# Kernel optimization log

Measured on AMD Instinct MI355X. Metric: run time of the kernel, lower is better.

The kernel has to match this reference:

```python
import jax, jax.numpy as jnp
import numpy as np

N_NODES = 50000
N_EDGES = 1200000
NODE_DIM = 64
HIDDEN = 64
OUT_DIM = 1
N_LAYERS = 3


def setup_inputs() -> dict:
    key = jax.random.key(0)
    ks = jax.random.split(key, 16)
    inp = {
        "H": jax.random.normal(ks[0], (N_NODES, NODE_DIM), dtype=jnp.float32),
        "edge_index": jax.random.randint(ks[1], (2, N_EDGES), 0, N_NODES, dtype=jnp.int64),
        "E": jax.random.normal(ks[2], (N_EDGES, 16), dtype=jnp.float32),
    }
    # per-layer params: node_encoder (enc) and update_w (upd); weights stored [in, out]
    for i in range(N_LAYERS):
        in_dim = NODE_DIM if i == 0 else HIDDEN
        s = 1.0 / np.sqrt(in_dim)
        inp[f"enc_w{i}"] = jax.random.uniform(ks[3 + 2 * i], (in_dim, HIDDEN), jnp.float32, -s, s)
        inp[f"enc_b{i}"] = jax.random.uniform(ks[4 + 2 * i], (HIDDEN,), jnp.float32, -s, s)
        sh = 1.0 / np.sqrt(HIDDEN)
        inp[f"upd_w{i}"] = jax.random.uniform(ks[9 + 2 * i], (HIDDEN, HIDDEN), jnp.float32, -sh, sh)
        inp[f"upd_b{i}"] = jax.random.uniform(ks[10 + 2 * i], (HIDDEN,), jnp.float32, -sh, sh)
    so = 1.0 / np.sqrt(HIDDEN)
    inp["out_w"] = jax.random.uniform(ks[15], (HIDDEN, OUT_DIM), jnp.float32, -so, so)
    inp["out_b"] = jnp.zeros((OUT_DIM,), jnp.float32)
    return inp


def _gcn_forward(H, edge_index, params):
    u, v = edge_index[0], edge_index[1]
    # symmetric normalization with implicit self-loop degree bump (calc_norm_factor)
    deg = jax.ops.segment_sum(jnp.ones(u.shape[0], H.dtype), u, num_segments=N_NODES) + 1.0
    dis = deg ** -0.5  # deg >= 1, never inf
    norm = dis[u] * dis[v]  # [n_edges]
    for i in range(N_LAYERS):
        enc_w, enc_b, upd_w, upd_b = params[i]
        H = H @ enc_w + enc_b                      # node_encoder
        msgs = norm[:, None] * H[u]                # gather + scale
        agg = jax.ops.segment_sum(msgs, v, num_segments=N_NODES)  # scatter-add
        H = jax.nn.relu((agg + H) @ upd_w + upd_b)  # update + ReLU (dropout = identity in eval)
    return H


def reference(H, edge_index, E, enc_w0, enc_b0, upd_w0, upd_b0, enc_w1, enc_b1,
              upd_w1, upd_b1, enc_w2, enc_b2, upd_w2, upd_b2, out_w, out_b):
    params = [(enc_w0, enc_b0, upd_w0, upd_b0),
              (enc_w1, enc_b1, upd_w1, upd_b1),
              (enc_w2, enc_b2, upd_w2, upd_b2)]
    Hf = _gcn_forward(H, edge_index, params)
    graph_emb = jnp.mean(Hf, axis=0, keepdims=True)  # [1, HIDDEN] readout (batch=None)
    return graph_emb @ out_w + out_b                 # [1, OUT_DIM]
```

## Files before the change

kernel.cpp:

```cpp
#include <hip/hip_runtime.h>
#include <hip/hip_fp16.h>

#define NN 50000
#define NE 1200000
#define DIM 64
#define NB 782
#define SLICES 512
#define ES 2344
#define VCAP 2048
#define GB 782
#define FRONT_LDS 33792


__device__ __forceinline__ void lsort_body(char* smem, const int* __restrict__ ei,
                                           ushort* __restrict__ usort,
                                           int* __restrict__ ebuf,
                                           int* __restrict__ lpart_u,
                                           int* __restrict__ lpart_v,
                                           int s) {
    int* hist = (int*)smem;
    int* wsum = (int*)(smem + 3136);
    ushort* sbu = (ushort*)(smem + 4160);
    int* sbv = (int*)(smem + 8848);
    int t = threadIdx.x;
    int w = t >> 6, l = t & 63;
    int e0 = s * ES, e1 = min(e0 + ES, NE), len = e1 - e0;
    int i0 = t * 4;

    int uv[10], vv[10];
#pragma unroll
    for (int j = 0; j < 10; ++j) {
        int e = e0 + t + j * 256;
        uv[j] = (e < e1) ? ei[e] : -1;
        vv[j] = (e < e1) ? ei[NE + e] : -1;
    }

    for (int i = t; i < NB; i += 256) hist[i] = 0;
    __syncthreads();
#pragma unroll
    for (int j = 0; j < 10; ++j)
        if (uv[j] >= 0) atomicAdd(&hist[uv[j] >> 6], 1);
    __syncthreads();
    {
        int h0 = (i0 + 0 < NB) ? hist[i0 + 0] : 0;
        int h1 = (i0 + 1 < NB) ? hist[i0 + 1] : 0;
        int h2 = (i0 + 2 < NB) ? hist[i0 + 2] : 0;
        int h3 = (i0 + 3 < NB) ? hist[i0 + 3] : 0;
        int p1 = h0, p2 = h0 + h1, p3 = p2 + h2, p4 = p3 + h3;
        int inc = p4;
        for (int o = 1; o < 64; o <<= 1) {
            int x = __shfl_up(inc, o, 64);
            if (l >= o) inc += x;
        }
        if (l == 63) wsum[w] = inc;
        __syncthreads();
        int base = 0;
#pragma unroll
        for (int j = 0; j < 4; ++j) if (j < w) base += wsum[j];
        int total = wsum[0] + wsum[1] + wsum[2] + wsum[3];
        int excl = base + inc - p4;
        int* lpu = lpart_u + s * (NB + 1);
        if (i0 + 0 < NB) { lpu[i0 + 0] = excl;      hist[i0 + 0] = excl; }
        if (i0 + 1 < NB) { lpu[i0 + 1] = excl + p1; hist[i0 + 1] = excl + p1; }
        if (i0 + 2 < NB) { lpu[i0 + 2] = excl + p2; hist[i0 + 2] = excl + p2; }
        if (i0 + 3 < NB) { lpu[i0 + 3] = excl + p3; hist[i0 + 3] = excl + p3; }
        if (t == 255) lpu[NB] = total;
    }
    __syncthreads();
#pragma unroll
    for (int j = 0; j < 10; ++j)
        if (uv[j] >= 0) {
            int pos = atomicAdd(&hist[uv[j] >> 6], 1);
            sbu[pos] = (ushort)uv[j];
        }
    __syncthreads();
    for (int i = t; i < len; i += 256) usort[e0 + i] = sbu[i];
    for (int i = t; i < NB; i += 256) hist[i] = 0;
    __syncthreads();

#pragma unroll
    for (int j = 0; j < 10; ++j)
        if (vv[j] >= 0) atomicAdd(&hist[vv[j] >> 6], 1);
    __syncthreads();
    {
        int h0 = (i0 + 0 < NB) ? hist[i0 + 0] : 0;
        int h1 = (i0 + 1 < NB) ? hist[i0 + 1] : 0;
        int h2 = (i0 + 2 < NB) ? hist[i0 + 2] : 0;
        int h3 = (i0 + 3 < NB) ? hist[i0 + 3] : 0;
        int p1 = h0, p2 = h0 + h1, p3 = p2 + h2, p4 = p3 + h3;
        int inc = p4;
        for (int o = 1; o < 64; o <<= 1) {
            int x = __shfl_up(inc, o, 64);
            if (l >= o) inc += x;
        }
        if (l == 63) wsum[w] = inc;
        __syncthreads();
        int base = 0;
#pragma unroll
        for (int j = 0; j < 4; ++j) if (j < w) base += wsum[j];
        int total = wsum[0] + wsum[1] + wsum[2] + wsum[3];
        int excl = base + inc - p4;
        int* lpv = lpart_v + s * (NB + 1);
        if (i0 + 0 < NB) { lpv[i0 + 0] = excl;      hist[i0 + 0] = excl; }
        if (i0 + 1 < NB) { lpv[i0 + 1] = excl + p1; hist[i0 + 1] = excl + p1; }
        if (i0 + 2 < NB) { lpv[i0 + 2] = excl + p2; hist[i0 + 2] = excl + p2; }
        if (i0 + 3 < NB) { lpv[i0 + 3] = excl + p3; hist[i0 + 3] = excl + p3; }
        if (t == 255) lpv[NB] = total;
    }
    __syncthreads();
#pragma unroll
    for (int j = 0; j < 10; ++j)
        if (vv[j] >= 0) {
            int pos = atomicAdd(&hist[vv[j] >> 6], 1);
            sbv[pos] = uv[j] | ((vv[j] & 63) << 16);
        }
    __syncthreads();
    for (int i = t; i < len; i += 256) ebuf[e0 + i] = sbv[i];
}

__device__ __forceinline__ void gemm_h_body(char* smem, int blk,
                                            const float* __restrict__ A,
                                            const float* __restrict__ W,
                                            const float* __restrict__ bias,
                                            __half* __restrict__ Ch, int M) {
    float (*As)[68] = (float(*)[68])smem;
    float (*Bs)[64] = (float(*)[64])(smem + 17408);
    int t = threadIdx.x;
    int row0 = blk * 64;
#pragma unroll
    for (int i = 0; i < 4; ++i) {
        int idx = t + i * 256;
        int r = idx >> 4, c = (idx & 15) << 2;
        float4 val = make_float4(0.f, 0.f, 0.f, 0.f);
        if (row0 + r < M) val = *(const float4*)&A[(size_t)(row0 + r) * DIM + c];
        *(float4*)&As[r][c] = val;
        *(float4*)&Bs[r][c] = *(const float4*)&W[r * DIM + c];
    }
    __syncthreads();
    int r0 = (t >> 4) * 4;
    int c0 = (t & 15) * 4;
    float acc[4][4] = {};
#pragma unroll
    for (int k = 0; k < 64; k += 4) {
        float4 b0 = *(float4*)&Bs[k + 0][c0];
        float4 b1 = *(float4*)&Bs[k + 1][c0];
        float4 b2 = *(float4*)&Bs[k + 2][c0];
        float4 b3 = *(float4*)&Bs[k + 3][c0];
#pragma unroll
        for (int i = 0; i < 4; ++i) {
            float4 av = *(float4*)&As[r0 + i][k];
            acc[i][0] = fmaf(av.x, b0.x, fmaf(av.y, b1.x, fmaf(av.z, b2.x, fmaf(av.w, b3.x, acc[i][0]))));
            acc[i][1] = fmaf(av.x, b0.y, fmaf(av.y, b1.y, fmaf(av.z, b2.y, fmaf(av.w, b3.y, acc[i][1]))));
            acc[i][2] = fmaf(av.x, b0.z, fmaf(av.y, b1.z, fmaf(av.z, b2.z, fmaf(av.w, b3.z, acc[i][2]))));
            acc[i][3] = fmaf(av.x, b0.w, fmaf(av.y, b1.w, fmaf(av.z, b2.w, fmaf(av.w, b3.w, acc[i][3]))));
        }
    }
    float4 bv = *(const float4*)&bias[c0];
#pragma unroll
    for (int i = 0; i < 4; ++i) {
        int r = row0 + r0 + i;
        if (r < M) {
            __half2 p0 = __floats2half2_rn(acc[i][0] + bv.x, acc[i][1] + bv.y);
            __half2 p1 = __floats2half2_rn(acc[i][2] + bv.z, acc[i][3] + bv.w);
            uint2 pk;
            pk.x = *(unsigned int*)&p0;
            pk.y = *(unsigned int*)&p1;
            *(uint2*)&Ch[(size_t)r * DIM + c0] = pk;
        }
    }
}

__global__ __launch_bounds__(256, 2) void k_front(const int* __restrict__ ei,
                                                  ushort* __restrict__ usort,
                                                  int* __restrict__ ebuf,
                                                  int* __restrict__ lpart_u,
                                                  int* __restrict__ lpart_v,
                                                  const float* __restrict__ A,
                                                  const float* __restrict__ W,
                                                  const float* __restrict__ bias,
                                                  __half* __restrict__ Ch) {
    extern __shared__ char smem[];
    int b = blockIdx.x;
    if (b < 256)
        lsort_body(smem, ei, usort, ebuf, lpart_u, lpart_v, b);
    else if (b < 512)
        gemm_h_body(smem, b - 256, A, W, bias, Ch, NN);
    else if (b < 768)
        lsort_body(smem, ei, usort, ebuf, lpart_u, lpart_v, b - 256);
    else
        gemm_h_body(smem, b - 512, A, W, bias, Ch, NN);
}

__global__ __launch_bounds__(256) void k_prep(const ushort* __restrict__ usort,
                                              const int* __restrict__ lpart_u,
                                              const int* __restrict__ ebuf,
                                              const int* __restrict__ lpart_v,
                                              float* __restrict__ dis,
                                              ushort* __restrict__ edges,
                                              int* __restrict__ row_ptr,
                                              float* __restrict__ colsum) {
    __shared__ int cache[VCAP];
    __shared__ int cnt[64];
    __shared__ int cur[64];
    __shared__ int wsum4[4];
    __shared__ int rsum4[4];
    __shared__ int sh[64];
    int bid = blockIdx.x;
    int t = threadIdx.x, w = t >> 6, l = t & 63;
    if (bid < NB) {
        int b = bid;
        if (b == 0 && t < 64) colsum[t] = 0.f;
        if (t < 64) sh[t] = 0;
        __syncthreads();
        for (int s = t; s < SLICES; s += 256) {
            const int* row = lpart_u + s * (NB + 1);
            int st = row[b], en = row[b + 1];
            for (int i = st; i < en; ++i)
                atomicAdd(&sh[usort[s * ES + i] & 63], 1);
        }
        __syncthreads();
        int n = (b << 6) + t;
        if (t < 64 && n < NN) dis[n] = rsqrtf((float)sh[t] + 1.0f);
        return;
    }
    int b = bid - NB;
    int s0 = t * 2, s1 = t * 2 + 1;
    const int* r0p = lpart_v + s0 * (NB + 1);
    const int* r1p = lpart_v + s1 * (NB + 1);
    int a0 = r0p[b], a1 = r0p[b + 1];
    int c0 = r1p[b], c1 = r1p[b + 1];
    int len0 = a1 - a0, len1 = c1 - c0;
    int tl = len0 + len1;
    int ts = a0 + c0;
    int inc = tl;
    for (int o = 1; o < 64; o <<= 1) {
        int x = __shfl_up(inc, o, 64);
        if (l >= o) inc += x;
    }
    int tss = ts;
    for (int off = 32; off; off >>= 1) tss += __shfl_down(tss, off, 64);
    if (l == 63) wsum4[w] = inc;
    if (l == 0) rsum4[w] = tss;
    if (t < 64) cnt[t] = 0;
    __syncthreads();
    int base = 0;
#pragma unroll
    for (int j = 0; j < 4; ++j) if (j < w) base += wsum4[j];
    int n = wsum4[0] + wsum4[1] + wsum4[2] + wsum4[3];
    int rbase = rsum4[0] + rsum4[1] + rsum4[2] + rsum4[3];
    int pos = base + inc - tl;
    if (n <= VCAP) {
        for (int i = 0; i < len0; ++i) cache[pos + i] = ebuf[s0 * ES + a0 + i];
        int pos1 = pos + len0;
        for (int i = 0; i < len1; ++i) cache[pos1 + i] = ebuf[s1 * ES + c0 + i];
        __syncthreads();
        for (int i = t; i < n; i += 256)
            atomicAdd(&cnt[(cache[i] >> 16) & 63], 1);
        __syncthreads();
        if (w == 0) {
            int c = cnt[l];
            int inc2 = c;
            for (int o = 1; o < 64; o <<= 1) {
                int x = __shfl_up(inc2, o, 64);
                if (l >= o) inc2 += x;
            }
            int excl = inc2 - c;
            cur[l] = rbase + excl;
            row_ptr[(b << 6) + l] = rbase + excl;
        }
        __syncthreads();
        for (int i = t; i < n; i += 256) {
            int rec = cache[i];
            int p2 = atomicAdd(&cur[(rec >> 16) & 63], 1);
            edges[p2] = (ushort)(rec & 0xFFFF);
        }
    } else {
        for (int s = t; s < SLICES; s += 256) {
            const int* row = lpart_v + s * (NB + 1);
            int st = row[b], en = row[b + 1];
            for (int i = st; i < en; ++i)
                atomicAdd(&cnt[(ebuf[s * ES + i] >> 16) & 63], 1);
        }
        __syncthreads();
        if (w == 0) {
            int c = cnt[l];
            int inc2 = c;
            for (int o = 1; o < 64; o <<= 1) {
                int x = __shfl_up(inc2, o, 64);
                if (l >= o) inc2 += x;
            }
            int excl = inc2 - c;
            cur[l] = rbase + excl;
            row_ptr[(b << 6) + l] = rbase + excl;
        }
        __syncthreads();
        for (int s = t; s < SLICES; s += 256) {
            const int* row = lpart_v + s * (NB + 1);
            int st = row[b], en = row[b + 1];
            for (int i = st; i < en; ++i) {
                int rec = ebuf[s * ES + i];
                int p2 = atomicAdd(&cur[(rec >> 16) & 63], 1);
                edges[p2] = (ushort)(rec & 0xFFFF);
            }
        }
    }
}

__global__ __launch_bounds__(256) void k_gemm2(const __half* __restrict__ Xh,
                                               const float* __restrict__ W1,
                                               const float* __restrict__ b1,
                                               const float* __restrict__ W2,
                                               const float* __restrict__ b2,
                                               __half* __restrict__ Zh, int M) {
    __shared__ float As[64][68];
    __shared__ float Bs[64][64];
    int t = threadIdx.x;
    int row0 = blockIdx.x * 64;
#pragma unroll
    for (int i = 0; i < 4; ++i) {
        int idx = t + i * 256;
        int r = idx >> 4, c = (idx & 15) << 2;
        float4 val = make_float4(0.f, 0.f, 0.f, 0.f);
        if (row0 + r < M) {
            uint2 hv = *(const uint2*)&Xh[(size_t)(row0 + r) * DIM + c];
            float2 f0 = __half22float2(*(const __half2*)&hv.x);
            float2 f1 = __half22float2(*(const __half2*)&hv.y);
            val = make_float4(f0.x, f0.y, f1.x, f1.y);
        }
        *(float4*)&As[r][c] = val;
        *(float4*)&Bs[r][c] = *(const float4*)&W1[r * DIM + c];
    }
    __syncthreads();
    int r0 = (t >> 4) * 4;
    int c0 = (t & 15) * 4;
    float acc[4][4] = {};
#pragma unroll
    for (int k = 0; k < 64; k += 4) {
        float4 v0 = *(float4*)&Bs[k + 0][c0];
        float4 v1 = *(float4*)&Bs[k + 1][c0];
        float4 v2 = *(float4*)&Bs[k + 2][c0];
        float4 v3 = *(float4*)&Bs[k + 3][c0];
#pragma unroll
        for (int i = 0; i < 4; ++i) {
            float4 av = *(float4*)&As[r0 + i][k];
            acc[i][0] = fmaf(av.x, v0.x, fmaf(av.y, v1.x, fmaf(av.z, v2.x, fmaf(av.w, v3.x, acc[i][0]))));
            acc[i][1] = fmaf(av.x, v0.y, fmaf(av.y, v1.y, fmaf(av.z, v2.y, fmaf(av.w, v3.y, acc[i][1]))));
            acc[i][2] = fmaf(av.x, v0.z, fmaf(av.y, v1.z, fmaf(av.z, v2.z, fmaf(av.w, v3.z, acc[i][2]))));
            acc[i][3] = fmaf(av.x, v0.w, fmaf(av.y, v1.w, fmaf(av.z, v2.w, fmaf(av.w, v3.w, acc[i][3]))));
        }
    }
    float4 bv1 = *(const float4*)&b1[c0];
    __syncthreads();
#pragma unroll
    for (int i = 0; i < 4; ++i) {
        float4 y;
        y.x = fmaxf(acc[i][0] + bv1.x, 0.f);
        y.y = fmaxf(acc[i][1] + bv1.y, 0.f);
        y.z = fmaxf(acc[i][2] + bv1.z, 0.f);
        y.w = fmaxf(acc[i][3] + bv1.w, 0.f);
        *(float4*)&As[r0 + i][c0] = y;
    }
#pragma unroll
    for (int i = 0; i < 4; ++i) {
        int idx = t + i * 256;
        int r = idx >> 4, c = (idx & 15) << 2;
        *(float4*)&Bs[r][c] = *(const float4*)&W2[r * DIM + c];
    }
    __syncthreads();
    float acc2[4][4] = {};
#pragma unroll
    for (int k = 0; k < 64; k += 4) {
        float4 v0 = *(float4*)&Bs[k + 0][c0];
        float4 v1 = *(float4*)&Bs[k + 1][c0];
        float4 v2 = *(float4*)&Bs[k + 2][c0];
        float4 v3 = *(float4*)&Bs[k + 3][c0];
#pragma unroll
        for (int i = 0; i < 4; ++i) {
            float4 av = *(float4*)&As[r0 + i][k];
            acc2[i][0] = fmaf(av.x, v0.x, fmaf(av.y, v1.x, fmaf(av.z, v2.x, fmaf(av.w, v3.x, acc2[i][0]))));
            acc2[i][1] = fmaf(av.x, v0.y, fmaf(av.y, v1.y, fmaf(av.z, v2.y, fmaf(av.w, v3.y, acc2[i][1]))));
            acc2[i][2] = fmaf(av.x, v0.z, fmaf(av.y, v1.z, fmaf(av.z, v2.z, fmaf(av.w, v3.z, acc2[i][2]))));
            acc2[i][3] = fmaf(av.x, v0.w, fmaf(av.y, v1.w, fmaf(av.z, v2.w, fmaf(av.w, v3.w, acc2[i][3]))));
        }
    }
    float4 bv2 = *(const float4*)&b2[c0];
#pragma unroll
    for (int i = 0; i < 4; ++i) {
        int r = row0 + r0 + i;
        if (r < M) {
            __half2 p0 = __floats2half2_rn(acc2[i][0] + bv2.x, acc2[i][1] + bv2.y);
            __half2 p1 = __floats2half2_rn(acc2[i][2] + bv2.z, acc2[i][3] + bv2.w);
            uint2 pk;
            pk.x = *(unsigned int*)&p0;
            pk.y = *(unsigned int*)&p1;
            *(uint2*)&Zh[(size_t)r * DIM + c0] = pk;
        }
    }
}

__global__ __launch_bounds__(256) void k_gemm_last(const __half* __restrict__ Xh,
                                                   const float* __restrict__ W,
                                                   const float* __restrict__ bias,
                                                   int M, float* __restrict__ colsum) {
    __shared__ float As[64][68];
    __shared__ float Bs[64][64];
    int t = threadIdx.x;
    int row0 = blockIdx.x * 64;
#pragma unroll
    for (int i = 0; i < 4; ++i) {
        int idx = t + i * 256;
        int r = idx >> 4, c = (idx & 15) << 2;
        float4 val = make_float4(0.f, 0.f, 0.f, 0.f);
        if (row0 + r < M) {
            uint2 hv = *(const uint2*)&Xh[(size_t)(row0 + r) * DIM + c];
            float2 f0 = __half22float2(*(const __half2*)&hv.x);
            float2 f1 = __half22float2(*(const __half2*)&hv.y);
            val = make_float4(f0.x, f0.y, f1.x, f1.y);
        }
        *(float4*)&As[r][c] = val;
        *(float4*)&Bs[r][c] = *(const float4*)&W[r * DIM + c];
    }
    __syncthreads();
    int r0 = (t >> 4) * 4;
    int c0 = (t & 15) * 4;
    float acc[4][4] = {};
#pragma unroll
    for (int k = 0; k < 64; k += 4) {
        float4 b0 = *(float4*)&Bs[k + 0][c0];
        float4 b1 = *(float4*)&Bs[k + 1][c0];
        float4 b2 = *(float4*)&Bs[k + 2][c0];
        float4 b3 = *(float4*)&Bs[k + 3][c0];
#pragma unroll
        for (int i = 0; i < 4; ++i) {
            float4 av = *(float4*)&As[r0 + i][k];
            acc[i][0] = fmaf(av.x, b0.x, fmaf(av.y, b1.x, fmaf(av.z, b2.x, fmaf(av.w, b3.x, acc[i][0]))));
            acc[i][1] = fmaf(av.x, b0.y, fmaf(av.y, b1.y, fmaf(av.z, b2.y, fmaf(av.w, b3.y, acc[i][1]))));
            acc[i][2] = fmaf(av.x, b0.z, fmaf(av.y, b1.z, fmaf(av.z, b2.z, fmaf(av.w, b3.z, acc[i][2]))));
            acc[i][3] = fmaf(av.x, b0.w, fmaf(av.y, b1.w, fmaf(av.z, b2.w, fmaf(av.w, b3.w, acc[i][3]))));
        }
    }
    float4 bv = *(const float4*)&bias[c0];
    float csum[4] = {0.f, 0.f, 0.f, 0.f};
#pragma unroll
    for (int i = 0; i < 4; ++i) {
        int r = row0 + r0 + i;
        if (r < M) {
            csum[0] += fmaxf(acc[i][0] + bv.x, 0.f);
            csum[1] += fmaxf(acc[i][1] + bv.y, 0.f);
            csum[2] += fmaxf(acc[i][2] + bv.z, 0.f);
            csum[3] += fmaxf(acc[i][3] + bv.w, 0.f);
        }
    }
    float* red = &As[0][0];
    __syncthreads();
    *(float4*)&red[(t >> 4) * 64 + c0] = make_float4(csum[0], csum[1], csum[2], csum[3]);
    __syncthreads();
    if (t < 64) {
        float s = 0.f;
#pragma unroll
        for (int g = 0; g < 16; ++g) s += red[g * 64 + t];
        atomicAdd(&colsum[t], s);
    }
}

__global__ __launch_bounds__(256) void k_agg(const uint4* __restrict__ Hq4,
                                             const float* __restrict__ dis,
                                             const int* __restrict__ row_ptr,
                                             const ushort* __restrict__ edges,
                                             __half* __restrict__ Xh) {
    __shared__ ushort se[4][64];
    __shared__ float swt[4][64];
    int w = threadIdx.x >> 6, l = threadIdx.x & 63;
    int node = (blockIdx.x << 2) + w;
    if (node >= NN) return;
    int start = row_ptr[node];
    int num = row_ptr[node + 1] - start;
    int g = l >> 3;
    int p = l & 7;
    float4 a0 = {0.f, 0.f, 0.f, 0.f};
    float4 a1 = {0.f, 0.f, 0.f, 0.f};
    for (int base = 0; base < num; base += 64) {
        int lim = min(64, num - base);
        ushort u = 0;
        float wv = 0.f;
        if (l < lim) { u = edges[start + base + l]; wv = dis[u]; }
        se[w][l] = u;
        swt[w][l] = wv;
        __builtin_amdgcn_wave_barrier();
        int octs = (lim + 7) >> 3;
        int rr[8]; float ww[8]; uint4 hh[8];
#pragma unroll
        for (int q = 0; q < 8; ++q)
            if (q < octs) { rr[q] = se[w][8 * q + g]; ww[q] = swt[w][8 * q + g]; }
#pragma unroll
        for (int q = 0; q < 8; ++q)
            if (q < octs) hh[q] = Hq4[(rr[q] << 3) + p];
#pragma unroll
        for (int q = 0; q < 8; ++q)
            if (q < octs) {
                float wt = ww[q];
                float2 f0 = __half22float2(*(const __half2*)&hh[q].x);
                float2 f1 = __half22float2(*(const __half2*)&hh[q].y);
                float2 f2 = __half22float2(*(const __half2*)&hh[q].z);
                float2 f3 = __half22float2(*(const __half2*)&hh[q].w);
                a0.x = fmaf(wt, f0.x, a0.x);
                a0.y = fmaf(wt, f0.y, a0.y);
                a0.z = fmaf(wt, f1.x, a0.z);
                a0.w = fmaf(wt, f1.y, a0.w);
                a1.x = fmaf(wt, f2.x, a1.x);
                a1.y = fmaf(wt, f2.y, a1.y);
                a1.z = fmaf(wt, f3.x, a1.z);
                a1.w = fmaf(wt, f3.y, a1.w);
            }
        __builtin_amdgcn_wave_barrier();
    }
#pragma unroll
    for (int m = 8; m < 64; m <<= 1) {
        a0.x += __shfl_xor(a0.x, m, 64);
        a0.y += __shfl_xor(a0.y, m, 64);
        a0.z += __shfl_xor(a0.z, m, 64);
        a0.w += __shfl_xor(a0.w, m, 64);
        a1.x += __shfl_xor(a1.x, m, 64);
        a1.y += __shfl_xor(a1.y, m, 64);
        a1.z += __shfl_xor(a1.z, m, 64);
        a1.w += __shfl_xor(a1.w, m, 64);
    }
    if (g == 0) {
        uint4 sv = Hq4[(node << 3) + p];
        float2 s0 = __half22float2(*(const __half2*)&sv.x);
        float2 s1 = __half22float2(*(const __half2*)&sv.y);
        float2 s2 = __half22float2(*(const __half2*)&sv.z);
        float2 s3 = __half22float2(*(const __half2*)&sv.w);
        float dv = dis[node];
        __half2 h0 = __floats2half2_rn(fmaf(dv, a0.x, s0.x), fmaf(dv, a0.y, s0.y));
        __half2 h1 = __floats2half2_rn(fmaf(dv, a0.z, s1.x), fmaf(dv, a0.w, s1.y));
        __half2 h2 = __floats2half2_rn(fmaf(dv, a1.x, s2.x), fmaf(dv, a1.y, s2.y));
        __half2 h3 = __floats2half2_rn(fmaf(dv, a1.z, s3.x), fmaf(dv, a1.w, s3.y));
        uint4 pk;
        pk.x = *(unsigned int*)&h0;
        pk.y = *(unsigned int*)&h1;
        pk.z = *(unsigned int*)&h2;
        pk.w = *(unsigned int*)&h3;
        *(uint4*)&Xh[((size_t)node << 6) + (p << 3)] = pk;
    }
}

__global__ void k_out(const float* __restrict__ colsum, const float* __restrict__ out_w,
                      const float* __restrict__ out_b, float* __restrict__ out) {
    int f = threadIdx.x;
    float v = colsum[f] * (1.0f / (float)NN) * out_w[f];
    for (int off = 32; off; off >>= 1) v += __shfl_down(v, off, 64);
    if (f == 0) out[0] = v + out_b[0];
}

extern "C" void kernel_launch(void* const* d_in, const int* in_sizes, int n_in,
                              void* d_out, int out_size, void* d_ws, size_t ws_size,
                              hipStream_t stream) {
    const float* H  = (const float*)d_in[0];
    const int*   ei = (const int*)d_in[1];
    const float* enc_w[3] = { (const float*)d_in[3], (const float*)d_in[7],  (const float*)d_in[11] };
    const float* enc_b[3] = { (const float*)d_in[4], (const float*)d_in[8],  (const float*)d_in[12] };
    const float* upd_w[3] = { (const float*)d_in[5], (const float*)d_in[9],  (const float*)d_in[13] };
    const float* upd_b[3] = { (const float*)d_in[6], (const float*)d_in[10], (const float*)d_in[14] };
    const float* out_w = (const float*)d_in[15];
    const float* out_b = (const float*)d_in[16];
    float* out = (float*)d_out;

    size_t off = 0;
    auto carve = [&](size_t bytes) {
        void* p = (char*)d_ws + off;
        off = (off + bytes + 255) & ~(size_t)255;
        return p;
    };
    int*    lpart_u = (int*)carve((size_t)SLICES * (NB + 1) * 4);
    int*    lpart_v = (int*)carve((size_t)SLICES * (NB + 1) * 4);
    float*  dis     = (float*)carve((size_t)NN * 4);
    ushort* usort   = (ushort*)carve((size_t)SLICES * ES * 2);
    int*    ebuf    = (int*)carve((size_t)SLICES * ES * 4);
    ushort* edges   = (ushort*)carve((size_t)NE * 2);
    int*    row_ptr = (int*)carve((size_t)(NN + 65) * 4);
    __half* Ch      = (__half*)carve((size_t)NN * DIM * 2);
    __half* Xh      = (__half*)carve((size_t)NN * DIM * 2);
    float*  colsum  = (float*)carve(64 * 4);

    const int AB = (NN + 3) / 4;
    const uint4* Hq4 = (const uint4*)Ch;

    k_front<<<512 + GB, 256, FRONT_LDS, stream>>>(ei, usort, ebuf, lpart_u, lpart_v,
                                                  H, enc_w[0], enc_b[0], Ch);
    k_prep<<<2 * NB, 256, 0, stream>>>(usort, lpart_u, ebuf, lpart_v,
                                       dis, edges, row_ptr, colsum);

    k_agg<<<AB, 256, 0, stream>>>(Hq4, dis, row_ptr, edges, Xh);
    k_gemm2<<<GB, 256, 0, stream>>>(Xh, upd_w[0], upd_b[0], enc_w[1], enc_b[1], Ch, NN);
    k_agg<<<AB, 256, 0, stream>>>(Hq4, dis, row_ptr, edges, Xh);
    k_gemm2<<<GB, 256, 0, stream>>>(Xh, upd_w[1], upd_b[1], enc_w[2], enc_b[2], Ch, NN);
    k_agg<<<AB, 256, 0, stream>>>(Hq4, dis, row_ptr, edges, Xh);
    k_gemm_last<<<GB, 256, 0, stream>>>(Xh, upd_w[2], upd_b[2], NN, colsum);

    k_out<<<1, 64, 0, stream>>>(colsum, out_w, out_b, out);
}
```

Baseline: 377.0 us.

## Fold encoder and update weights into one matrix per layer, fuse ReLU into aggregation

Precomputes Wp = enc_w @ upd_w and bias vectors per layer in a small kernel. Each layer then does a single GEMM, P = H @ Wp, followed by aggregation that applies the folded bias via a per-node weight sum s and the ReLU in its epilogue. This replaces the old chained two-GEMM kernel and removes one GEMM pass per layer. The final per-column reduction moves to a separate colsum kernel. Extra costs are a per-node s array, small per-layer vector loads in aggregation, and fp16 rounding of the folded product, which may change accuracy.

```diff
diff --git a/kernel.cpp b/kernel.cpp
--- a/kernel.cpp
+++ b/kernel.cpp
@@ -10,6 +10,60 @@
 #define VCAP 2048
 #define GB 782
 #define FRONT_LDS 33792
+
+__global__ __launch_bounds__(256) void k_fold(const float* __restrict__ E0, const float* __restrict__ e0,
+                                              const float* __restrict__ U0, const float* __restrict__ ub0,
+                                              const float* __restrict__ E1, const float* __restrict__ e1,
+                                              const float* __restrict__ U1, const float* __restrict__ ub1,
+                                              const float* __restrict__ E2, const float* __restrict__ e2,
+                                              const float* __restrict__ U2, const float* __restrict__ ub2,
+                                              float* __restrict__ Wp, float* __restrict__ cvec,
+                                              float* __restrict__ dvec) {
+    __shared__ float Es[64][64];
+    __shared__ float Us[64][64];
+    int i = blockIdx.x;
+    const float* E  = (i == 0) ? E0  : (i == 1) ? E1  : E2;
+    const float* e  = (i == 0) ? e0  : (i == 1) ? e1  : e2;
+    const float* U  = (i == 0) ? U0  : (i == 1) ? U1  : U2;
+    const float* ub = (i == 0) ? ub0 : (i == 1) ? ub1 : ub2;
+    int t = threadIdx.x;
+#pragma unroll
+    for (int j = 0; j < 4; ++j) {
+        int idx = t + j * 256;
+        int r = idx >> 4, c = (idx & 15) << 2;
+        *(float4*)&Es[r][c] = *(const float4*)&E[r * 64 + c];
+        *(float4*)&Us[r][c] = *(const float4*)&U[r * 64 + c];
+    }
+    __syncthreads();
+    int r0 = (t >> 4) * 4;
+    int c0 = (t & 15) * 4;
+    float acc[4][4] = {};
+#pragma unroll
+    for (int k = 0; k < 64; k += 4) {
+        float4 b0 = *(float4*)&Us[k + 0][c0];
+        float4 b1 = *(float4*)&Us[k + 1][c0];
+        float4 b2 = *(float4*)&Us[k + 2][c0];
+        float4 b3 = *(float4*)&Us[k + 3][c0];
+#pragma unroll
+        for (int q = 0; q < 4; ++q) {
+            float4 av = *(float4*)&Es[r0 + q][k];
+            acc[q][0] = fmaf(av.x, b0.x, fmaf(av.y, b1.x, fmaf(av.z, b2.x, fmaf(av.w, b3.x, acc[q][0]))));
+            acc[q][1] = fmaf(av.x, b0.y, fmaf(av.y, b1.y, fmaf(av.z, b2.y, fmaf(av.w, b3.y, acc[q][1]))));
+            acc[q][2] = fmaf(av.x, b0.z, fmaf(av.y, b1.z, fmaf(av.z, b2.z, fmaf(av.w, b3.z, acc[q][2]))));
+            acc[q][3] = fmaf(av.x, b0.w, fmaf(av.y, b1.w, fmaf(av.z, b2.w, fmaf(av.w, b3.w, acc[q][3]))));
+        }
+    }
+    float* W = Wp + i * 4096;
+#pragma unroll
+    for (int q = 0; q < 4; ++q)
+        *(float4*)&W[(r0 + q) * 64 + c0] = make_float4(acc[q][0], acc[q][1], acc[q][2], acc[q][3]);
+    if (t < 64) {
+        float sc = 0.f;
+        for (int k = 0; k < 64; ++k) sc = fmaf(e[k], Us[k][t], sc);
+        cvec[i * 64 + t] = sc;
+        dvec[i * 64 + t] = sc + ub[t];
+    }
+}
 
 
 __device__ __forceinline__ void lsort_body(char* smem, const int* __restrict__ ei,
@@ -121,8 +175,7 @@
 __device__ __forceinline__ void gemm_h_body(char* smem, int blk,
                                             const float* __restrict__ A,
                                             const float* __restrict__ W,
-                                            const float* __restrict__ bias,
-                                            __half* __restrict__ Ch, int M) {
+                                            __half* __restrict__ Ph, int M) {
     float (*As)[68] = (float(*)[68])smem;
     float (*Bs)[64] = (float(*)[64])(smem + 17408);
     int t = threadIdx.x;
@@ -155,17 +208,16 @@
             acc[i][3] = fmaf(av.x, b0.w, fmaf(av.y, b1.w, fmaf(av.z, b2.w, fmaf(av.w, b3.w, acc[i][3]))));
         }
     }
-    float4 bv = *(const float4*)&bias[c0];
 #pragma unroll
     for (int i = 0; i < 4; ++i) {
         int r = row0 + r0 + i;
         if (r < M) {
-            __half2 p0 = __floats2half2_rn(acc[i][0] + bv.x, acc[i][1] + bv.y);
-            __half2 p1 = __floats2half2_rn(acc[i][2] + bv.z, acc[i][3] + bv.w);
+            __half2 p0 = __floats2half2_rn(acc[i][0], acc[i][1]);
+            __half2 p1 = __floats2half2_rn(acc[i][2], acc[i][3]);
             uint2 pk;
             pk.x = *(unsigned int*)&p0;
             pk.y = *(unsigned int*)&p1;
-            *(uint2*)&Ch[(size_t)r * DIM + c0] = pk;
+            *(uint2*)&Ph[(size_t)r * DIM + c0] = pk;
         }
     }
 }
@@ -176,19 +228,18 @@
                                                   int* __restrict__ lpart_u,
                                                   int* __restrict__ lpart_v,
                                                   const float* __restrict__ A,
-                                                  const float* __restrict__ W,
-                                                  const float* __restrict__ bias,
-                                                  __half* __restrict__ Ch) {
+                                                  const float* __restrict__ Wp,
+                                                  __half* __restrict__ Ph) {
     extern __shared__ char smem[];
     int b = blockIdx.x;
     if (b < 256)
         lsort_body(smem, ei, usort, ebuf, lpart_u, lpart_v, b);
     else if (b < 512)
-        gemm_h_body(smem, b - 256, A, W, bias, Ch, NN);
+        gemm_h_body(smem, b - 256, A, Wp, Ph, NN);
     else if (b < 768)
         lsort_body(smem, ei, usort, ebuf, lpart_u, lpart_v, b - 256);
     else
-        gemm_h_body(smem, b - 512, A, W, bias, Ch, NN);
+        gemm_h_body(smem, b - 512, A, Wp, Ph, NN);
 }
 
 __global__ __launch_bounds__(256) void k_prep(const ushort* __restrict__ usort,
@@ -306,12 +357,9 @@
     }
 }
 
-__global__ __launch_bounds__(256) void k_gemm2(const __half* __restrict__ Xh,
-                                               const float* __restrict__ W1,
-                                               const float* __restrict__ b1,
-                                               const float* __restrict__ W2,
-                                               const float* __restrict__ b2,
-                                               __half* __restrict__ Zh, int M) {
+__global__ __launch_bounds__(256) void k_gemm(const __half* __restrict__ Hh,
+                                              const float* __restrict__ W,
+                                              __half* __restrict__ Ph) {
     __shared__ float As[64][68];
     __shared__ float Bs[64][64];
     int t = threadIdx.x;
@@ -321,98 +369,8 @@
         int idx = t + i * 256;
         int r = idx >> 4, c = (idx & 15) << 2;
         float4 val = make_float4(0.f, 0.f, 0.f, 0.f);
-        if (row0 + r < M) {
-            uint2 hv = *(const uint2*)&Xh[(size_t)(row0 + r) * DIM + c];
-            float2 f0 = __half22float2(*(const __half2*)&hv.x);
-            float2 f1 = __half22float2(*(const __half2*)&hv.y);
-            val = make_float4(f0.x, f0.y, f1.x, f1.y);
-        }
-        *(float4*)&As[r][c] = val;
-        *(float4*)&Bs[r][c] = *(const float4*)&W1[r * DIM + c];
-    }
-    __syncthreads();
-    int r0 = (t >> 4) * 4;
-    int c0 = (t & 15) * 4;
-    float acc[4][4] = {};
-#pragma unroll
-    for (int k = 0; k < 64; k += 4) {
-        float4 v0 = *(float4*)&Bs[k + 0][c0];
-        float4 v1 = *(float4*)&Bs[k + 1][c0];
-        float4 v2 = *(float4*)&Bs[k + 2][c0];
-        float4 v3 = *(float4*)&Bs[k + 3][c0];
-#pragma unroll
-        for (int i = 0; i < 4; ++i) {
-            float4 av = *(float4*)&As[r0 + i][k];
-            acc[i][0] = fmaf(av.x, v0.x, fmaf(av.y, v1.x, fmaf(av.z, v2.x, fmaf(av.w, v3.x, acc[i][0]))));
-            acc[i][1] = fmaf(av.x, v0.y, fmaf(av.y, v1.y, fmaf(av.z, v2.y, fmaf(av.w, v3.y, acc[i][1]))));
-            acc[i][2] = fmaf(av.x, v0.z, fmaf(av.y, v1.z, fmaf(av.z, v2.z, fmaf(av.w, v3.z, acc[i][2]))));
-            acc[i][3] = fmaf(av.x, v0.w, fmaf(av.y, v1.w, fmaf(av.z, v2.w, fmaf(av.w, v3.w, acc[i][3]))));
-        }
-    }
-    float4 bv1 = *(const float4*)&b1[c0];
-    __syncthreads();
-#pragma unroll
-    for (int i = 0; i < 4; ++i) {
-        float4 y;
-        y.x = fmaxf(acc[i][0] + bv1.x, 0.f);
-        y.y = fmaxf(acc[i][1] + bv1.y, 0.f);
-        y.z = fmaxf(acc[i][2] + bv1.z, 0.f);
-        y.w = fmaxf(acc[i][3] + bv1.w, 0.f);
-        *(float4*)&As[r0 + i][c0] = y;
-    }
-#pragma unroll
-    for (int i = 0; i < 4; ++i) {
-        int idx = t + i * 256;
-        int r = idx >> 4, c = (idx & 15) << 2;
-        *(float4*)&Bs[r][c] = *(const float4*)&W2[r * DIM + c];
-    }
-    __syncthreads();
-    float acc2[4][4] = {};
-#pragma unroll
-    for (int k = 0; k < 64; k += 4) {
-        float4 v0 = *(float4*)&Bs[k + 0][c0];
-        float4 v1 = *(float4*)&Bs[k + 1][c0];
-        float4 v2 = *(float4*)&Bs[k + 2][c0];
-        float4 v3 = *(float4*)&Bs[k + 3][c0];
-#pragma unroll
-        for (int i = 0; i < 4; ++i) {
-            float4 av = *(float4*)&As[r0 + i][k];
-            acc2[i][0] = fmaf(av.x, v0.x, fmaf(av.y, v1.x, fmaf(av.z, v2.x, fmaf(av.w, v3.x, acc2[i][0]))));
-            acc2[i][1] = fmaf(av.x, v0.y, fmaf(av.y, v1.y, fmaf(av.z, v2.y, fmaf(av.w, v3.y, acc2[i][1]))));
-            acc2[i][2] = fmaf(av.x, v0.z, fmaf(av.y, v1.z, fmaf(av.z, v2.z, fmaf(av.w, v3.z, acc2[i][2]))));
-            acc2[i][3] = fmaf(av.x, v0.w, fmaf(av.y, v1.w, fmaf(av.z, v2.w, fmaf(av.w, v3.w, acc2[i][3]))));
-        }
-    }
-    float4 bv2 = *(const float4*)&b2[c0];
-#pragma unroll
-    for (int i = 0; i < 4; ++i) {
-        int r = row0 + r0 + i;
-        if (r < M) {
-            __half2 p0 = __floats2half2_rn(acc2[i][0] + bv2.x, acc2[i][1] + bv2.y);
-            __half2 p1 = __floats2half2_rn(acc2[i][2] + bv2.z, acc2[i][3] + bv2.w);
-            uint2 pk;
-            pk.x = *(unsigned int*)&p0;
-            pk.y = *(unsigned int*)&p1;
-            *(uint2*)&Zh[(size_t)r * DIM + c0] = pk;
-        }
-    }
-}
-
-__global__ __launch_bounds__(256) void k_gemm_last(const __half* __restrict__ Xh,
-                                                   const float* __restrict__ W,
-                                                   const float* __restrict__ bias,
-                                                   int M, float* __restrict__ colsum) {
-    __shared__ float As[64][68];
-    __shared__ float Bs[64][64];
-    int t = threadIdx.x;
-    int row0 = blockIdx.x * 64;
-#pragma unroll
-    for (int i = 0; i < 4; ++i) {
-        int idx = t + i * 256;
-        int r = idx >> 4, c = (idx & 15) << 2;
-        float4 val = make_float4(0.f, 0.f, 0.f, 0.f);
-        if (row0 + r < M) {
-            uint2 hv = *(const uint2*)&Xh[(size_t)(row0 + r) * DIM + c];
+        if (row0 + r < NN) {
+            uint2 hv = *(const uint2*)&Hh[(size_t)(row0 + r) * DIM + c];
             float2 f0 = __half22float2(*(const __half2*)&hv.x);
             float2 f1 = __half22float2(*(const __half2*)&hv.y);
             val = make_float4(f0.x, f0.y, f1.x, f1.y);
@@ -439,46 +397,40 @@
             acc[i][3] = fmaf(av.x, b0.w, fmaf(av.y, b1.w, fmaf(av.z, b2.w, fmaf(av.w, b3.w, acc[i][3]))));
         }
     }
-    float4 bv = *(const float4*)&bias[c0];
-    float csum[4] = {0.f, 0.f, 0.f, 0.f};
 #pragma unroll
     for (int i = 0; i < 4; ++i) {
         int r = row0 + r0 + i;
-        if (r < M) {
-            csum[0] += fmaxf(acc[i][0] + bv.x, 0.f);
-            csum[1] += fmaxf(acc[i][1] + bv.y, 0.f);
-            csum[2] += fmaxf(acc[i][2] + bv.z, 0.f);
-            csum[3] += fmaxf(acc[i][3] + bv.w, 0.f);
-        }
-    }
-    float* red = &As[0][0];
-    __syncthreads();
-    *(float4*)&red[(t >> 4) * 64 + c0] = make_float4(csum[0], csum[1], csum[2], csum[3]);
-    __syncthreads();
-    if (t < 64) {
-        float s = 0.f;
-#pragma unroll
-        for (int g = 0; g < 16; ++g) s += red[g * 64 + t];
-        atomicAdd(&colsum[t], s);
-    }
-}
-
-__global__ __launch_bounds__(256) void k_agg(const uint4* __restrict__ Hq4,
+        if (r < NN) {
+            __half2 p0 = __floats2half2_rn(acc[i][0], acc[i][1]);
+            __half2 p1 = __floats2half2_rn(acc[i][2], acc[i][3]);
+            uint2 pk;
+            pk.x = *(unsigned int*)&p0;
+            pk.y = *(unsigned int*)&p1;
+            *(uint2*)&Ph[(size_t)r * DIM + c0] = pk;
+        }
+    }
+}
+
+template<bool FIRST>
+__global__ __launch_bounds__(256) void k_agg(const uint4* __restrict__ Pq4,
                                              const float* __restrict__ dis,
                                              const int* __restrict__ row_ptr,
                                              const ushort* __restrict__ edges,
-                                             __half* __restrict__ Xh) {
+                                             const float* __restrict__ cvec,
+                                             const float* __restrict__ dvec,
+                                             float* __restrict__ s,
+                                             __half* __restrict__ Hh) {
     __shared__ ushort se[4][64];
     __shared__ float swt[4][64];
     int w = threadIdx.x >> 6, l = threadIdx.x & 63;
     int node = (blockIdx.x << 2) + w;
-    if (node >= NN) return;
     int start = row_ptr[node];
     int num = row_ptr[node + 1] - start;
     int g = l >> 3;
     int p = l & 7;
     float4 a0 = {0.f, 0.f, 0.f, 0.f};
     float4 a1 = {0.f, 0.f, 0.f, 0.f};
+    float sw = 0.f;
     for (int base = 0; base < num; base += 64) {
         int lim = min(64, num - base);
         ushort u = 0;
@@ -494,11 +446,12 @@
             if (q < octs) { rr[q] = se[w][8 * q + g]; ww[q] = swt[w][8 * q + g]; }
 #pragma unroll
         for (int q = 0; q < 8; ++q)
-            if (q < octs) hh[q] = Hq4[(rr[q] << 3) + p];
+            if (q < octs) hh[q] = Pq4[(rr[q] << 3) + p];
 #pragma unroll
         for (int q = 0; q < 8; ++q)
             if (q < octs) {
                 float wt = ww[q];
+                if (FIRST) sw += wt;
                 float2 f0 = __half22float2(*(const __half2*)&hh[q].x);
                 float2 f1 = __half22float2(*(const __half2*)&hh[q].y);
                 float2 f2 = __half22float2(*(const __half2*)&hh[q].z);
@@ -524,25 +477,68 @@
         a1.y += __shfl_xor(a1.y, m, 64);
         a1.z += __shfl_xor(a1.z, m, 64);
         a1.w += __shfl_xor(a1.w, m, 64);
+        if (FIRST) sw += __shfl_xor(sw, m, 64);
     }
     if (g == 0) {
-        uint4 sv = Hq4[(node << 3) + p];
-        float2 s0 = __half22float2(*(const __half2*)&sv.x);
-        float2 s1 = __half22float2(*(const __half2*)&sv.y);
-        float2 s2 = __half22float2(*(const __half2*)&sv.z);
-        float2 s3 = __half22float2(*(const __half2*)&sv.w);
         float dv = dis[node];
-        __half2 h0 = __floats2half2_rn(fmaf(dv, a0.x, s0.x), fmaf(dv, a0.y, s0.y));
-        __half2 h1 = __floats2half2_rn(fmaf(dv, a0.z, s1.x), fmaf(dv, a0.w, s1.y));
-        __half2 h2 = __floats2half2_rn(fmaf(dv, a1.x, s2.x), fmaf(dv, a1.y, s2.y));
-        __half2 h3 = __floats2half2_rn(fmaf(dv, a1.z, s3.x), fmaf(dv, a1.w, s3.y));
+        float sv;
+        if (FIRST) {
+            sv = dv * sw;
+            if (p == 0) s[node] = sv;
+        } else {
+            sv = s[node];
+        }
+        uint4 pv = Pq4[(node << 3) + p];
+        float2 s0 = __half22float2(*(const __half2*)&pv.x);
+        float2 s1 = __half22float2(*(const __half2*)&pv.y);
+        float2 s2 = __half22float2(*(const __half2*)&pv.z);
+        float2 s3 = __half22float2(*(const __half2*)&pv.w);
+        float4 cA = *(const float4*)&cvec[p << 3];
+        float4 cB = *(const float4*)&cvec[(p << 3) + 4];
+        float4 dA = *(const float4*)&dvec[p << 3];
+        float4 dB = *(const float4*)&dvec[(p << 3) + 4];
+        float o0 = fmaxf(fmaf(dv, a0.x, s0.x) + fmaf(sv, cA.x, dA.x), 0.f);
+        float o1 = fmaxf(fmaf(dv, a0.y, s0.y) + fmaf(sv, cA.y, dA.y), 0.f);
+        float o2 = fmaxf(fmaf(dv, a0.z, s1.x) + fmaf(sv, cA.z, dA.z), 0.f);
+        float o3 = fmaxf(fmaf(dv, a0.w, s1.y) + fmaf(sv, cA.w, dA.w), 0.f);
+        float o4 = fmaxf(fmaf(dv, a1.x, s2.x) + fmaf(sv, cB.x, dB.x), 0.f);
+        float o5 = fmaxf(fmaf(dv, a1.y, s2.y) + fmaf(sv, cB.y, dB.y), 0.f);
+        float o6 = fmaxf(fmaf(dv, a1.z, s3.x) + fmaf(sv, cB.z, dB.z), 0.f);
+        float o7 = fmaxf(fmaf(dv, a1.w, s3.y) + fmaf(sv, cB.w, dB.w), 0.f);
+        __half2 h0 = __floats2half2_rn(o0, o1);
+        __half2 h1 = __floats2half2_rn(o2, o3);
+        __half2 h2 = __floats2half2_rn(o4, o5);
+        __half2 h3 = __floats2half2_rn(o6, o7);
         uint4 pk;
         pk.x = *(unsigned int*)&h0;
         pk.y = *(unsigned int*)&h1;
         pk.z = *(unsigned int*)&h2;
         pk.w = *(unsigned int*)&h3;
-        *(uint4*)&Xh[((size_t)node << 6) + (p << 3)] = pk;
-    }
+        *(uint4*)&Hh[((size_t)node << 6) + (p << 3)] = pk;
+    }
+}
+
+__global__ __launch_bounds__(256) void k_colsum(const __half* __restrict__ Hh,
+                                                float* __restrict__ colsum) {
+    __shared__ float scs[64];
+    int t = threadIdx.x;
+    if (t < 64) scs[t] = 0.f;
+    __syncthreads();
+    int p = t & 7;
+    float a[8] = {};
+    for (int r = blockIdx.x * 32 + (t >> 3); r < NN; r += 256 * 32) {
+        uint4 hv = *(const uint4*)&Hh[((size_t)r << 6) + (p << 3)];
+        float2 f0 = __half22float2(*(const __half2*)&hv.x);
+        float2 f1 = __half22float2(*(const __half2*)&hv.y);
+        float2 f2 = __half22float2(*(const __half2*)&hv.z);
+        float2 f3 = __half22float2(*(const __half2*)&hv.w);
+        a[0] += f0.x; a[1] += f0.y; a[2] += f1.x; a[3] += f1.y;
+        a[4] += f2.x; a[5] += f2.y; a[6] += f3.x; a[7] += f3.y;
+    }
+#pragma unroll
+    for (int j = 0; j < 8; ++j) atomicAdd(&scs[(p << 3) + j], a[j]);
+    __syncthreads();
+    if (t < 64) atomicAdd(&colsum[t], scs[t]);
 }
 
 __global__ void k_out(const float* __restrict__ colsum, const float* __restrict__ out_w,
@@ -575,28 +571,39 @@
     int*    lpart_u = (int*)carve((size_t)SLICES * (NB + 1) * 4);
     int*    lpart_v = (int*)carve((size_t)SLICES * (NB + 1) * 4);
     float*  dis     = (float*)carve((size_t)NN * 4);
+    float*  sarr    = (float*)carve((size_t)NN * 4);
     ushort* usort   = (ushort*)carve((size_t)SLICES * ES * 2);
     int*    ebuf    = (int*)carve((size_t)SLICES * ES * 4);
     ushort* edges   = (ushort*)carve((size_t)NE * 2);
     int*    row_ptr = (int*)carve((size_t)(NN + 65) * 4);
-    __half* Ch      = (__half*)carve((size_t)NN * DIM * 2);
-    __half* Xh      = (__half*)carve((size_t)NN * DIM * 2);
+    __half* Ph      = (__half*)carve((size_t)NN * DIM * 2);
+    __half* Hh      = (__half*)carve((size_t)NN * DIM * 2);
+    float*  Wp      = (float*)carve(3 * 64 * 64 * 4);
+    float*  cvec    = (float*)carve(3 * 64 * 4);
+    float*  dvec    = (float*)carve(3 * 64 * 4);
     float*  colsum  = (float*)carve(64 * 4);
 
-    const int AB = (NN + 3) / 4;
-    const uint4* Hq4 = (const uint4*)Ch;
-
+    const int AB = NN / 4;
+    const uint4* Pq4 = (const uint4*)Ph;
+
+    k_fold<<<3, 256, 0, stream>>>(enc_w[0], enc_b[0], upd_w[0], upd_b[0],
+                                  enc_w[1], enc_b[1], upd_w[1], upd_b[1],
+                                  enc_w[2], enc_b[2], upd_w[2], upd_b[2],
+                                  Wp, cvec, dvec);
     k_front<<<512 + GB, 256, FRONT_LDS, stream>>>(ei, usort, ebuf, lpart_u, lpart_v,
-                                                  H, enc_w[0], enc_b[0], Ch);
+                                                  H, Wp, Ph);
     k_prep<<<2 * NB, 256, 0, stream>>>(usort, lpart_u, ebuf, lpart_v,
                                        dis, edges, row_ptr, colsum);
 
-    k_agg<<<AB, 256, 0, stream>>>(Hq4, dis, row_ptr, edges, Xh);
-    k_gemm2<<<GB, 256, 0, stream>>>(Xh, upd_w[0], upd_b[0], enc_w[1], enc_b[1], Ch, NN);
-    k_agg<<<AB, 256, 0, stream>>>(Hq4, dis, row_ptr, edges, Xh);
-    k_gemm2<<<GB, 256, 0, stream>>>(Xh, upd_w[1], upd_b[1], enc_w[2], enc_b[2], Ch, NN);
-    k_agg<<<AB, 256, 0, stream>>>(Hq4, dis, row_ptr, edges, Xh);
-    k_gemm_last<<<GB, 256, 0, stream>>>(Xh, upd_w[2], upd_b[2], NN, colsum);
-
+    k_agg<true><<<AB, 256, 0, stream>>>(Pq4, dis, row_ptr, edges,
+                                        cvec + 0, dvec + 0, sarr, Hh);
+    k_gemm<<<GB, 256, 0, stream>>>(Hh, Wp + 4096, Ph);
+    k_agg<false><<<AB, 256, 0, stream>>>(Pq4, dis, row_ptr, edges,
+                                         cvec + 64, dvec + 64, sarr, Hh);
+    k_gemm<<<GB, 256, 0, stream>>>(Hh, Wp + 8192, Ph);
+    k_agg<false><<<AB, 256, 0, stream>>>(Pq4, dis, row_ptr, edges,
+                                         cvec + 128, dvec + 128, sarr, Hh);
+
+    k_colsum<<<256, 256, 0, stream>>>(Hh, colsum);
     k_out<<<1, 64, 0, stream>>>(colsum, out_w, out_b, out);
 }
```

Result: faster. 342.2 us (-9.2%).
